# Kernel optimization log

Measured on AMD Instinct MI355X. Metric: run time of the kernel, lower is better.

The kernel has to match this reference:

```python
import jax, jax.numpy as jnp
import numpy as np

OFFSETS = (1, 2, 4, 8)
N, C, H, E = 256, 512, 256, 4


def _layer_norm(x, w, b, eps=1e-5):
    mu = x.mean(-1, keepdims=True)
    var = ((x - mu) ** 2).mean(-1, keepdims=True)
    return (x - mu) / jnp.sqrt(var + eps) * w + b


def _linear_init(key, fan_in, fan_out):
    k1, k2 = jax.random.split(key)
    bound = 1.0 / np.sqrt(fan_in)
    w = jax.random.uniform(k1, (fan_in, fan_out), jnp.float32, -bound, bound)
    b = jax.random.uniform(k2, (fan_out,), jnp.float32, -bound, bound)
    return w, b


def setup_inputs() -> dict:
    key = jax.random.key(0)
    ks = jax.random.split(key, 8)
    h = jax.random.normal(ks[0], (N, C, H), jnp.float32)
    xyz = jax.random.normal(ks[1], (N, C, 3), jnp.float32) * 10.0
    valid = jax.random.randint(ks[2], (N, C), 0, 2).astype(bool)
    # msg_mlp: Linear(2H+E -> 2H), GELU, Linear(2H -> H)
    w1, b1 = _linear_init(ks[3], 2 * H + E, 2 * H)
    w2, b2 = _linear_init(ks[4], 2 * H, H)
    # update ResidualMLP: LN(H), Linear(H -> 4H), GELU, Linear(4H -> H)
    u1, bu1 = _linear_init(ks[5], H, 4 * H)
    u2, bu2 = _linear_init(ks[6], 4 * H, H)
    return {
        "h": h, "xyz": xyz, "valid": valid,
        "ln_n_w": jnp.ones((H,), jnp.float32), "ln_n_b": jnp.zeros((H,), jnp.float32),
        "w1": w1, "b1": b1, "w2": w2, "b2": b2,
        "ln_u_w": jnp.ones((H,), jnp.float32), "ln_u_b": jnp.zeros((H,), jnp.float32),
        "u1": u1, "bu1": bu1, "u2": u2, "bu2": bu2,
    }


def _msg_mlp(x, w1, b1, w2, b2):
    y = jax.nn.gelu(x @ w1 + b1, approximate=False)
    return y @ w2 + b2


def reference(h, xyz, valid, ln_n_w, ln_n_b, w1, b1, w2, b2,
              ln_u_w, ln_u_b, u1, bu1, u2, bu2):
    n, c, hd = h.shape
    h_in = _layer_norm(h, ln_n_w, ln_n_b)
    valid_f = valid.astype(h.dtype)[..., None]  # [N, C, 1]
    agg = jnp.zeros_like(h_in)
    for off in OFFSETS:
        if off >= c:
            continue
        # dst = [0, c-off), src = [off, c)
        h_i = h_in[:, : c - off]
        h_j = h_in[:, off:]
        v = (valid[:, off:] & valid[:, : c - off]).astype(h.dtype)[..., None]
        delta = xyz[:, off:] - xyz[:, : c - off]  # xyz_j - xyz_i
        dist = jnp.maximum(jnp.linalg.norm(delta, axis=-1, keepdims=True), 1e-6)
        unit = delta / dist
        e_fwd = jnp.concatenate([unit, dist], axis=-1)
        msg_fwd = _msg_mlp(jnp.concatenate([h_i, h_j, e_fwd], axis=-1), w1, b1, w2, b2)
        agg = agg.at[:, : c - off].add(msg_fwd * v)
        e_rev = jnp.concatenate([-unit, dist], axis=-1)
        msg_rev = _msg_mlp(jnp.concatenate([h_j, h_i, e_rev], axis=-1), w1, b1, w2, b2)
        agg = agg.at[:, off:].add(msg_rev * v)
    h = h + agg * valid_f
    # ResidualMLP update
    hu = _layer_norm(h, ln_u_w, ln_u_b)
    hu = jax.nn.gelu(hu @ u1 + bu1, approximate=False) @ u2 + bu2
    h = (h + hu) * valid_f
    return h
```

## Files before the change

### kernel.cpp

```cpp
#include <hip/hip_runtime.h>
#include <stdint.h>

typedef unsigned short u16;
typedef __attribute__((ext_vector_type(8))) short short8v;
typedef __attribute__((ext_vector_type(4))) short short4v;
typedef __attribute__((ext_vector_type(4))) float f32x4;

#define CC 512
#define HD 256

__device__ __forceinline__ u16 f2bf(float f) {
  union { float f; uint32_t u; } v; v.f = f;
  return (u16)((v.u + 0x7FFFu + ((v.u >> 16) & 1u)) >> 16);
}
__device__ __forceinline__ float bf2f(u16 h) {
  union { uint32_t u; float f; } v; v.u = ((uint32_t)h) << 16;
  return v.f;
}
__device__ __forceinline__ float gelu_c(float x) {
  float x2 = x * x;
  float a  = x * fmaf(x2, 0.044715f, 1.0f);
  float t  = __builtin_amdgcn_exp2f(a * -2.3022118f);
  return x * __builtin_amdgcn_rcpf(1.0f + t);
}

__global__ void prep_weights(const float* __restrict__ w1, const float* __restrict__ w2,
                             const float* __restrict__ u1, const float* __restrict__ u2,
                             u16* __restrict__ ws) {
  int idx = blockIdx.x * blockDim.x + threadIdx.x;
  if (idx >= 917504) return;
  float val;
  if (idx < 131072)      { int n = idx >> 8, k = idx & 255; val = w1[k * 512 + n]; }
  else if (idx < 262144) { int i = idx - 131072, n = i >> 8, k = i & 255; val = w1[(256 + k) * 512 + n]; }
  else if (idx < 393216) { int i = idx - 262144, n = i >> 9, k = i & 511; val = w2[k * 256 + n]; }
  else if (idx < 655360) { int i = idx - 393216, n = i >> 8, k = i & 255; val = u1[k * 1024 + n]; }
  else                   { int i = idx - 655360, n = i >> 10, k = i & 1023; val = u2[k * 256 + n]; }
  ws[idx] = f2bf(val);
}

#define SPQ 520
#define SHS 264
#define Q_OFF   0
#define P_OFF   33280
#define H_OFF   49920
#define W1E_OFF 66816
#define B1_OFF  75008
#define EX_OFF  77056
#define NV_OFF  79616
#define STRIP_LDS 79680

__global__ __launch_bounds__(512) void strip_kernel(
    const float* __restrict__ hin, const float* __restrict__ xyz, const int* __restrict__ valid,
    const float* __restrict__ lnw, const float* __restrict__ lnb,
    const float* __restrict__ w1, const float* __restrict__ b1,
    const u16* __restrict__ WaT, const u16* __restrict__ WbT,
    const u16* __restrict__ W2T, const float* __restrict__ b2,
    float* __restrict__ out) {
  extern __shared__ char lds[];
  u16* sQ   = (u16*)(lds + Q_OFF);
  u16* sP   = (u16*)(lds + P_OFF);
  u16* sH   = (u16*)(lds + H_OFF);
  u16* sAct = (u16*)(lds + H_OFF);
  float* sW1e = (float*)(lds + W1E_OFF);
  float* sB1  = (float*)(lds + B1_OFF);
  float* sEx  = (float*)(lds + EX_OFF);
  float* sEy = sEx + 128; float* sEz = sEx + 256;
  float* sEd = sEx + 384; float* sV  = sEx + 512;
  float* sNV = (float*)(lds + NV_OFF);

  const int tid  = threadIdx.x;
  const int lane = tid & 63;
  const int wid  = tid >> 6;
  const int quad = lane >> 4;
  const int l16  = lane & 15;
  const int n    = blockIdx.y;
  const int c0   = blockIdx.x * 16;

  for (int i = tid; i < 2048; i += 512) sW1e[i] = w1[262144 + i];
  sB1[tid] = b1[tid];

  if (tid < 128) {
    const int p = tid >> 4, r = tid & 15;
    const int off = 1 << (p >> 1);
    const bool fwd = ((p & 1) == 0);
    const int c = c0 + r;
    const int other = fwd ? (c + off) : (c - off);
    const bool inb = (other >= 0) && (other < CC);
    const int oc = inb ? other : c;
    float vv = 0.f;
    if (inb && (valid[n * CC + c] != 0) && (valid[n * CC + oc] != 0)) vv = 1.f;
    const float* xo = xyz + (size_t)(n * CC + oc) * 3;
    const float* xc = xyz + (size_t)(n * CC + c) * 3;
    const float dx = xo[0] - xc[0], dy = xo[1] - xc[1], dz = xo[2] - xc[2];
    const float dist = fmaxf(sqrtf(dx*dx + dy*dy + dz*dz), 1e-6f);
    const float rin = 1.f / dist;
    sEx[tid] = dx * rin; sEy[tid] = dy * rin; sEz[tid] = dz * rin;
    sEd[tid] = dist; sV[tid] = vv;
  }

  for (int i = 0; i < 4; ++i) {
    const int r = wid * 4 + i;
    const int ch = c0 - 8 + r;
    float x0 = 0.f, x1 = 0.f, x2 = 0.f, x3 = 0.f;
    if (ch >= 0 && ch < CC) {
      const float* src = hin + (size_t)(n * CC + ch) * HD + lane * 4;
      x0 = src[0]; x1 = src[1]; x2 = src[2]; x3 = src[3];
    }
    float s = x0 + x1 + x2 + x3;
    float ss = x0*x0 + x1*x1 + x2*x2 + x3*x3;
    #pragma unroll
    for (int m = 1; m < 64; m <<= 1) { s += __shfl_xor(s, m, 64); ss += __shfl_xor(ss, m, 64); }
    const float mu = s * (1.f / 256.f);
    const float rstd = rsqrtf(ss * (1.f / 256.f) - mu * mu + 1e-5f);
    const int k4 = lane * 4;
    short4v pk;
    ((u16*)&pk)[0] = f2bf((x0 - mu) * rstd * lnw[k4 + 0] + lnb[k4 + 0]);
    ((u16*)&pk)[1] = f2bf((x1 - mu) * rstd * lnw[k4 + 1] + lnb[k4 + 1]);
    ((u16*)&pk)[2] = f2bf((x2 - mu) * rstd * lnw[k4 + 2] + lnb[k4 + 2]);
    ((u16*)&pk)[3] = f2bf((x3 - mu) * rstd * lnw[k4 + 3] + lnb[k4 + 3]);
    *(short4v*)&sH[r * SHS + k4] = pk;
  }
  __syncthreads();

  if (tid < 16) {
    float s = 0.f;
    #pragma unroll
    for (int p = 0; p < 8; ++p) s += sV[p * 16 + tid];
    sNV[tid] = s;
  }
  for (int nt = wid; nt < 32; nt += 8) {
    const int col = nt * 16 + l16;
    short8v bw[8];
    {
      const u16* bp = WaT + (size_t)col * 256;
      #pragma unroll
      for (int ks = 0; ks < 8; ++ks) bw[ks] = *(const short8v*)(bp + ks * 32 + quad * 8);
      const u16* ar = sH + (8 + l16) * SHS;
      f32x4 acc = {0.f, 0.f, 0.f, 0.f};
      #pragma unroll
      for (int ks = 0; ks < 8; ++ks)
        acc = __builtin_amdgcn_mfma_f32_16x16x32_bf16(*(const short8v*)(ar + ks * 32 + quad * 8), bw[ks], acc, 0, 0, 0);
      #pragma unroll
      for (int r = 0; r < 4; ++r) sP[(quad * 4 + r) * SPQ + col] = f2bf(acc[r]);
    }
    {
      const u16* bp = WbT + (size_t)col * 256;
      #pragma unroll
      for (int ks = 0; ks < 8; ++ks) bw[ks] = *(const short8v*)(bp + ks * 32 + quad * 8);
      #pragma unroll
      for (int mt = 0; mt < 2; ++mt) {
        const u16* ar = sH + (mt * 16 + l16) * SHS;
        f32x4 acc = {0.f, 0.f, 0.f, 0.f};
        #pragma unroll
        for (int ks = 0; ks < 8; ++ks)
          acc = __builtin_amdgcn_mfma_f32_16x16x32_bf16(*(const short8v*)(ar + ks * 32 + quad * 8), bw[ks], acc, 0, 0, 0);
        #pragma unroll
        for (int r = 0; r < 4; ++r) sQ[(mt * 16 + quad * 4 + r) * SPQ + col] = f2bf(acc[r]);
      }
    }
  }
  __syncthreads();

  const int row = tid >> 5;
  const int kl  = tid & 31;
  float accr[4][4];
  #pragma unroll
  for (int b = 0; b < 4; ++b)
    #pragma unroll
    for (int j = 0; j < 4; ++j) accr[b][j] = 0.f;
  short4v pp[4];
  {
    const u16* pr = sP + row * SPQ;
    #pragma unroll
    for (int b = 0; b < 4; ++b) pp[b] = *(const short4v*)(pr + kl * 4 + b * 128);
  }
  for (int pass = 0; pass < 8; ++pass) {
    const float vv = sV[pass * 16 + row];
    if (vv != 0.f) {
      const int off = 1 << (pass >> 1);
      const int doff = (pass & 1) ? -off : off;
      const float ex = sEx[pass * 16 + row], ey = sEy[pass * 16 + row];
      const float ez = sEz[pass * 16 + row], ed = sEd[pass * 16 + row];
      const u16* qr = sQ + (row + 8 + doff) * SPQ;
      #pragma unroll
      for (int b = 0; b < 4; ++b) {
        const int k0 = kl * 4 + b * 128;
        short4v qq = *(const short4v*)(qr + k0);
        const float4 we0 = *(const float4*)&sW1e[k0];
        const float4 we1 = *(const float4*)&sW1e[512 + k0];
        const float4 we2 = *(const float4*)&sW1e[1024 + k0];
        const float4 we3 = *(const float4*)&sW1e[1536 + k0];
        const float4 bb  = *(const float4*)&sB1[k0];
        #pragma unroll
        for (int j = 0; j < 4; ++j) {
          float pre = bf2f(((u16*)&pp[b])[j]) + bf2f(((u16*)&qq)[j])
                    + ex * ((const float*)&we0)[j] + ey * ((const float*)&we1)[j]
                    + ez * ((const float*)&we2)[j] + ed * ((const float*)&we3)[j]
                    + ((const float*)&bb)[j];
          accr[b][j] += gelu_c(pre);
        }
      }
    }
  }
  __syncthreads();
  {
    u16* aw = sAct + row * SPQ;
    #pragma unroll
    for (int b = 0; b < 4; ++b) {
      short4v pk;
      #pragma unroll
      for (int j = 0; j < 4; ++j) ((u16*)&pk)[j] = f2bf(accr[b][j]);
      *(short4v*)(aw + kl * 4 + b * 128) = pk;
    }
  }
  __syncthreads();

  {
    const int nt0 = wid * 2, nt1 = wid * 2 + 1;
    const u16* b0p = W2T + (size_t)(nt0 * 16 + l16) * 512;
    const u16* b1p = W2T + (size_t)(nt1 * 16 + l16) * 512;
    f32x4 a0 = {0.f, 0.f, 0.f, 0.f}, a1 = {0.f, 0.f, 0.f, 0.f};
    #pragma unroll
    for (int ks = 0; ks < 16; ++ks) {
      short8v a = *(const short8v*)(sAct + l16 * SPQ + ks * 32 + quad * 8);
      a0 = __builtin_amdgcn_mfma_f32_16x16x32_bf16(a, *(const short8v*)(b0p + ks * 32 + quad * 8), a0, 0, 0, 0);
      a1 = __builtin_amdgcn_mfma_f32_16x16x32_bf16(a, *(const short8v*)(b1p + ks * 32 + quad * 8), a1, 0, 0, 0);
    }
    #pragma unroll
    for (int t = 0; t < 2; ++t) {
      const f32x4 av = t ? a1 : a0;
      const int col = (t ? nt1 : nt0) * 16 + l16;
      const float b2v = b2[col];
      #pragma unroll
      for (int r = 0; r < 4; ++r) {
        const int rw = quad * 4 + r;
        const int gc = c0 + rw;
        const float vown = (valid[n * CC + gc] != 0) ? 1.f : 0.f;
        const size_t gi = (size_t)(n * CC + gc) * HD + col;
        out[gi] = hin[gi] + (av[r] + b2v * sNV[rw]) * vown;
      }
    }
  }
}

#define X_S 264
#define Y_S 520
#define UX_OFF 0
#define UY_OFF 16896
#define UPD_LDS 50176

__global__ __launch_bounds__(512) void update_kernel(
    const float* __restrict__ lnw, const float* __restrict__ lnb,
    const u16* __restrict__ U1T, const float* __restrict__ bu1,
    const u16* __restrict__ U2T, const float* __restrict__ bu2,
    const int* __restrict__ valid, float* __restrict__ out) {
  extern __shared__ char lds[];
  u16* sX = (u16*)(lds + UX_OFF);
  u16* sY = (u16*)(lds + UY_OFF);

  const int tid  = threadIdx.x;
  const int lane = tid & 63;
  const int wid  = tid >> 6;
  const int quad = lane >> 4;
  const int l16  = lane & 15;
  const int n    = blockIdx.y;
  const int c0   = blockIdx.x * 32;

  for (int i = 0; i < 4; ++i) {
    const int r = wid * 4 + i;
    const int k4 = lane * 4;
    const float* src = out + (size_t)(n * CC + c0 + r) * HD + k4;
    const float x0 = src[0], x1 = src[1], x2 = src[2], x3 = src[3];
    float s = x0 + x1 + x2 + x3;
    float ss = x0*x0 + x1*x1 + x2*x2 + x3*x3;
    #pragma unroll
    for (int m = 1; m < 64; m <<= 1) { s += __shfl_xor(s, m, 64); ss += __shfl_xor(ss, m, 64); }
    const float mu = s * (1.f / 256.f);
    const float rstd = rsqrtf(ss * (1.f / 256.f) - mu * mu + 1e-5f);
    short4v pk;
    ((u16*)&pk)[0] = f2bf((x0 - mu) * rstd * lnw[k4 + 0] + lnb[k4 + 0]);
    ((u16*)&pk)[1] = f2bf((x1 - mu) * rstd * lnw[k4 + 1] + lnb[k4 + 1]);
    ((u16*)&pk)[2] = f2bf((x2 - mu) * rstd * lnw[k4 + 2] + lnb[k4 + 2]);
    ((u16*)&pk)[3] = f2bf((x3 - mu) * rstd * lnw[k4 + 3] + lnb[k4 + 3]);
    *(short4v*)&sX[r * X_S + k4] = pk;
  }
  __syncthreads();

  const int nt0 = wid * 2, nt1 = wid * 2 + 1;
  f32x4 acc2[2][2];
  #pragma unroll
  for (int a = 0; a < 2; ++a)
    #pragma unroll
    for (int b = 0; b < 2; ++b) acc2[a][b] = (f32x4){0.f, 0.f, 0.f, 0.f};

  for (int half = 0; half < 2; ++half) {
    if (half) __syncthreads();
    for (int j = 0; j < 4; ++j) {
      const int nt = wid + j * 8;
      const int nrow = half * 512 + nt * 16 + l16;
      short8v bw[8];
      const u16* bp = U1T + (size_t)nrow * 256;
      #pragma unroll
      for (int ks = 0; ks < 8; ++ks) bw[ks] = *(const short8v*)(bp + ks * 32 + quad * 8);
      const float bv = bu1[nrow];
      #pragma unroll
      for (int mt = 0; mt < 2; ++mt) {
        const u16* ar = sX + (mt * 16 + l16) * X_S;
        f32x4 acc = {0.f, 0.f, 0.f, 0.f};
        #pragma unroll
        for (int ks = 0; ks < 8; ++ks)
          acc = __builtin_amdgcn_mfma_f32_16x16x32_bf16(*(const short8v*)(ar + ks * 32 + quad * 8), bw[ks], acc, 0, 0, 0);
        #pragma unroll
        for (int r = 0; r < 4; ++r)
          sY[(mt * 16 + quad * 4 + r) * Y_S + nt * 16 + l16] = f2bf(gelu_c(acc[r] + bv));
      }
    }
    __syncthreads();
    const u16* b0p = U2T + (size_t)(nt0 * 16 + l16) * 1024 + half * 512;
    const u16* b1p = U2T + (size_t)(nt1 * 16 + l16) * 1024 + half * 512;
    #pragma unroll
    for (int ks = 0; ks < 16; ++ks) {
      short8v aA = *(const short8v*)(sY + l16 * Y_S + ks * 32 + quad * 8);
      short8v aB = *(const short8v*)(sY + (16 + l16) * Y_S + ks * 32 + quad * 8);
      short8v b0 = *(const short8v*)(b0p + ks * 32 + quad * 8);
      short8v b1 = *(const short8v*)(b1p + ks * 32 + quad * 8);
      acc2[0][0] = __builtin_amdgcn_mfma_f32_16x16x32_bf16(aA, b0, acc2[0][0], 0, 0, 0);
      acc2[1][0] = __builtin_amdgcn_mfma_f32_16x16x32_bf16(aB, b0, acc2[1][0], 0, 0, 0);
      acc2[0][1] = __builtin_amdgcn_mfma_f32_16x16x32_bf16(aA, b1, acc2[0][1], 0, 0, 0);
      acc2[1][1] = __builtin_amdgcn_mfma_f32_16x16x32_bf16(aB, b1, acc2[1][1], 0, 0, 0);
    }
  }

  #pragma unroll
  for (int mt = 0; mt < 2; ++mt) {
    #pragma unroll
    for (int t = 0; t < 2; ++t) {
      const int col = (t ? nt1 : nt0) * 16 + l16;
      const float bv = bu2[col];
      #pragma unroll
      for (int r = 0; r < 4; ++r) {
        const int rw = mt * 16 + quad * 4 + r;
        const int gc = c0 + rw;
        const float vown = (valid[n * CC + gc] != 0) ? 1.f : 0.f;
        const size_t gi = (size_t)(n * CC + gc) * HD + col;
        out[gi] = (out[gi] + acc2[mt][t][r] + bv) * vown;
      }
    }
  }
}

extern "C" void kernel_launch(void* const* d_in, const int* in_sizes, int n_in,
                              void* d_out, int out_size, void* d_ws, size_t ws_size,
                              hipStream_t stream) {
  (void)in_sizes; (void)n_in; (void)out_size; (void)ws_size;
  const float* h     = (const float*)d_in[0];
  const float* xyz   = (const float*)d_in[1];
  const int*   valid = (const int*)d_in[2];
  const float* lnnw  = (const float*)d_in[3];
  const float* lnnb  = (const float*)d_in[4];
  const float* w1    = (const float*)d_in[5];
  const float* b1    = (const float*)d_in[6];
  const float* w2    = (const float*)d_in[7];
  const float* b2    = (const float*)d_in[8];
  const float* lnuw  = (const float*)d_in[9];
  const float* lnub  = (const float*)d_in[10];
  const float* u1    = (const float*)d_in[11];
  const float* bu1   = (const float*)d_in[12];
  const float* u2    = (const float*)d_in[13];
  const float* bu2   = (const float*)d_in[14];
  float* out = (float*)d_out;
  u16* ws = (u16*)d_ws;

  hipFuncSetAttribute(reinterpret_cast<const void*>(strip_kernel),
                      hipFuncAttributeMaxDynamicSharedMemorySize, STRIP_LDS);
  hipFuncSetAttribute(reinterpret_cast<const void*>(update_kernel),
                      hipFuncAttributeMaxDynamicSharedMemorySize, UPD_LDS);

  prep_weights<<<dim3(3584), dim3(256), 0, stream>>>(w1, w2, u1, u2, ws);
  strip_kernel<<<dim3(32, 256), dim3(512), STRIP_LDS, stream>>>(
      h, xyz, valid, lnnw, lnnb, w1, b1, ws, ws + 131072, ws + 262144, b2, out);
  update_kernel<<<dim3(16, 256), dim3(512), UPD_LDS, stream>>>(
      lnuw, lnub, ws + 393216, bu1, ws + 655360, bu2, valid, out);
}
```

Before: 1.511 ms.

## Fuse strip message kernel with residual MLP update kernel via LDS handoff

Merges the message-passing strip kernel and the residual-MLP update kernel into one kernel. The intermediate h is kept in LDS instead of being written to global memory and read back. The b1 bias is folded into the P projection, and edge weights are held in registers rather than LDS, which shrinks LDS use and targets 4 blocks per CU. The cost is that the update MLP now runs on 16-row tiles, so each U1/U2 weight fetch is reused across half as many rows, and register pressure rises.

```diff
diff --git a/kernel.cpp b/kernel.cpp
--- a/kernel.cpp
+++ b/kernel.cpp
@@ -40,30 +40,33 @@
 
 #define SPQ 520
 #define SHS 264
+#define OUTS 260
 #define Q_OFF   0
 #define P_OFF   33280
 #define H_OFF   49920
-#define W1E_OFF 66816
-#define B1_OFF  75008
-#define EX_OFF  77056
-#define NV_OFF  79616
-#define STRIP_LDS 79680
-
-__global__ __launch_bounds__(512) void strip_kernel(
+#define E_OFF   66816
+#define NV_OFF  69376
+#define FUSED_LDS 69440
+
+__global__ __launch_bounds__(512, 4) void fused_kernel(
     const float* __restrict__ hin, const float* __restrict__ xyz, const int* __restrict__ valid,
     const float* __restrict__ lnw, const float* __restrict__ lnb,
     const float* __restrict__ w1, const float* __restrict__ b1,
     const u16* __restrict__ WaT, const u16* __restrict__ WbT,
     const u16* __restrict__ W2T, const float* __restrict__ b2,
+    const float* __restrict__ lnuw, const float* __restrict__ lnub,
+    const u16* __restrict__ U1T, const float* __restrict__ bu1,
+    const u16* __restrict__ U2T, const float* __restrict__ bu2,
     float* __restrict__ out) {
   extern __shared__ char lds[];
   u16* sQ   = (u16*)(lds + Q_OFF);
   u16* sP   = (u16*)(lds + P_OFF);
   u16* sH   = (u16*)(lds + H_OFF);
   u16* sAct = (u16*)(lds + H_OFF);
-  float* sW1e = (float*)(lds + W1E_OFF);
-  float* sB1  = (float*)(lds + B1_OFF);
-  float* sEx  = (float*)(lds + EX_OFF);
+  float* sOut = (float*)(lds + P_OFF);
+  u16* sX   = (u16*)(lds + Q_OFF);
+  u16* sY   = (u16*)(lds + Q_OFF + 8448);
+  float* sEx = (float*)(lds + E_OFF);
   float* sEy = sEx + 128; float* sEz = sEx + 256;
   float* sEd = sEx + 384; float* sV  = sEx + 512;
   float* sNV = (float*)(lds + NV_OFF);
@@ -75,9 +78,7 @@
   const int l16  = lane & 15;
   const int n    = blockIdx.y;
   const int c0   = blockIdx.x * 16;
-
-  for (int i = tid; i < 2048; i += 512) sW1e[i] = w1[262144 + i];
-  sB1[tid] = b1[tid];
+  const int k4   = lane * 4;
 
   if (tid < 128) {
     const int p = tid >> 4, r = tid & 15;
@@ -98,27 +99,30 @@
     sEd[tid] = dist; sV[tid] = vv;
   }
 
-  for (int i = 0; i < 4; ++i) {
-    const int r = wid * 4 + i;
-    const int ch = c0 - 8 + r;
-    float x0 = 0.f, x1 = 0.f, x2 = 0.f, x3 = 0.f;
-    if (ch >= 0 && ch < CC) {
-      const float* src = hin + (size_t)(n * CC + ch) * HD + lane * 4;
-      x0 = src[0]; x1 = src[1]; x2 = src[2]; x3 = src[3];
-    }
-    float s = x0 + x1 + x2 + x3;
-    float ss = x0*x0 + x1*x1 + x2*x2 + x3*x3;
-    #pragma unroll
-    for (int m = 1; m < 64; m <<= 1) { s += __shfl_xor(s, m, 64); ss += __shfl_xor(ss, m, 64); }
-    const float mu = s * (1.f / 256.f);
-    const float rstd = rsqrtf(ss * (1.f / 256.f) - mu * mu + 1e-5f);
-    const int k4 = lane * 4;
-    short4v pk;
-    ((u16*)&pk)[0] = f2bf((x0 - mu) * rstd * lnw[k4 + 0] + lnb[k4 + 0]);
-    ((u16*)&pk)[1] = f2bf((x1 - mu) * rstd * lnw[k4 + 1] + lnb[k4 + 1]);
-    ((u16*)&pk)[2] = f2bf((x2 - mu) * rstd * lnw[k4 + 2] + lnb[k4 + 2]);
-    ((u16*)&pk)[3] = f2bf((x3 - mu) * rstd * lnw[k4 + 3] + lnb[k4 + 3]);
-    *(short4v*)&sH[r * SHS + k4] = pk;
+  {
+    const float4 lw = *(const float4*)&lnw[k4];
+    const float4 lb = *(const float4*)&lnb[k4];
+    for (int i = 0; i < 4; ++i) {
+      const int r = wid * 4 + i;
+      const int ch = c0 - 8 + r;
+      float x0 = 0.f, x1 = 0.f, x2 = 0.f, x3 = 0.f;
+      if (ch >= 0 && ch < CC) {
+        const float* src = hin + (size_t)(n * CC + ch) * HD + k4;
+        x0 = src[0]; x1 = src[1]; x2 = src[2]; x3 = src[3];
+      }
+      float s = x0 + x1 + x2 + x3;
+      float ss = x0*x0 + x1*x1 + x2*x2 + x3*x3;
+      #pragma unroll
+      for (int m = 1; m < 64; m <<= 1) { s += __shfl_xor(s, m, 64); ss += __shfl_xor(ss, m, 64); }
+      const float mu = s * (1.f / 256.f);
+      const float rstd = rsqrtf(ss * (1.f / 256.f) - mu * mu + 1e-5f);
+      short4v pk;
+      ((u16*)&pk)[0] = f2bf((x0 - mu) * rstd * lw.x + lb.x);
+      ((u16*)&pk)[1] = f2bf((x1 - mu) * rstd * lw.y + lb.y);
+      ((u16*)&pk)[2] = f2bf((x2 - mu) * rstd * lw.z + lb.z);
+      ((u16*)&pk)[3] = f2bf((x3 - mu) * rstd * lw.w + lb.w);
+      *(short4v*)&sH[r * SHS + k4] = pk;
+    }
   }
   __syncthreads();
 
@@ -140,8 +144,9 @@
       #pragma unroll
       for (int ks = 0; ks < 8; ++ks)
         acc = __builtin_amdgcn_mfma_f32_16x16x32_bf16(*(const short8v*)(ar + ks * 32 + quad * 8), bw[ks], acc, 0, 0, 0);
-      #pragma unroll
-      for (int r = 0; r < 4; ++r) sP[(quad * 4 + r) * SPQ + col] = f2bf(acc[r]);
+      const float bias = b1[col];
+      #pragma unroll
+      for (int r = 0; r < 4; ++r) sP[(quad * 4 + r) * SPQ + col] = f2bf(acc[r] + bias);
     }
     {
       const u16* bp = WbT + (size_t)col * 256;
@@ -163,47 +168,45 @@
 
   const int row = tid >> 5;
   const int kl  = tid & 31;
-  float accr[4][4];
-  #pragma unroll
-  for (int b = 0; b < 4; ++b)
-    #pragma unroll
-    for (int j = 0; j < 4; ++j) accr[b][j] = 0.f;
-  short4v pp[4];
   {
-    const u16* pr = sP + row * SPQ;
-    #pragma unroll
-    for (int b = 0; b < 4; ++b) pp[b] = *(const short4v*)(pr + kl * 4 + b * 128);
-  }
-  for (int pass = 0; pass < 8; ++pass) {
-    const float vv = sV[pass * 16 + row];
-    if (vv != 0.f) {
-      const int off = 1 << (pass >> 1);
-      const int doff = (pass & 1) ? -off : off;
-      const float ex = sEx[pass * 16 + row], ey = sEy[pass * 16 + row];
-      const float ez = sEz[pass * 16 + row], ed = sEd[pass * 16 + row];
-      const u16* qr = sQ + (row + 8 + doff) * SPQ;
-      #pragma unroll
-      for (int b = 0; b < 4; ++b) {
-        const int k0 = kl * 4 + b * 128;
-        short4v qq = *(const short4v*)(qr + k0);
-        const float4 we0 = *(const float4*)&sW1e[k0];
-        const float4 we1 = *(const float4*)&sW1e[512 + k0];
-        const float4 we2 = *(const float4*)&sW1e[1024 + k0];
-        const float4 we3 = *(const float4*)&sW1e[1536 + k0];
-        const float4 bb  = *(const float4*)&sB1[k0];
+    short4v pp[4];
+    float4 we[4][4];
+    #pragma unroll
+    for (int b = 0; b < 4; ++b) pp[b] = *(const short4v*)(sP + row * SPQ + kl * 4 + b * 128);
+    #pragma unroll
+    for (int d = 0; d < 4; ++d)
+      #pragma unroll
+      for (int b = 0; b < 4; ++b)
+        we[d][b] = *(const float4*)&w1[(size_t)(512 + d) * 512 + kl * 4 + b * 128];
+    float accr[4][4];
+    #pragma unroll
+    for (int b = 0; b < 4; ++b)
+      #pragma unroll
+      for (int j = 0; j < 4; ++j) accr[b][j] = 0.f;
+
+    for (int pass = 0; pass < 8; ++pass) {
+      const float vv = sV[pass * 16 + row];
+      if (vv != 0.f) {
+        const int off = 1 << (pass >> 1);
+        const int doff = (pass & 1) ? -off : off;
+        const float ex = sEx[pass * 16 + row], ey = sEy[pass * 16 + row];
+        const float ez = sEz[pass * 16 + row], ed = sEd[pass * 16 + row];
+        const u16* qr = sQ + (row + 8 + doff) * SPQ;
         #pragma unroll
-        for (int j = 0; j < 4; ++j) {
-          float pre = bf2f(((u16*)&pp[b])[j]) + bf2f(((u16*)&qq)[j])
-                    + ex * ((const float*)&we0)[j] + ey * ((const float*)&we1)[j]
-                    + ez * ((const float*)&we2)[j] + ed * ((const float*)&we3)[j]
-                    + ((const float*)&bb)[j];
-          accr[b][j] += gelu_c(pre);
+        for (int b = 0; b < 4; ++b) {
+          short4v qq = *(const short4v*)(qr + kl * 4 + b * 128);
+          #pragma unroll
+          for (int j = 0; j < 4; ++j) {
+            float et = ex * ((const float*)&we[0][b])[j];
+            et = fmaf(ey, ((const float*)&we[1][b])[j], et);
+            et = fmaf(ez, ((const float*)&we[2][b])[j], et);
+            et = fmaf(ed, ((const float*)&we[3][b])[j], et);
+            const float pre = bf2f(((const u16*)&pp[b])[j]) + bf2f(((const u16*)&qq)[j]) + et;
+            accr[b][j] += gelu_c(pre);
+          }
         }
       }
     }
-  }
-  __syncthreads();
-  {
     u16* aw = sAct + row * SPQ;
     #pragma unroll
     for (int b = 0; b < 4; ++b) {
@@ -215,8 +218,8 @@
   }
   __syncthreads();
 
+  const int nt0 = wid * 2, nt1 = wid * 2 + 1;
   {
-    const int nt0 = wid * 2, nt1 = wid * 2 + 1;
     const u16* b0p = W2T + (size_t)(nt0 * 16 + l16) * 512;
     const u16* b1p = W2T + (size_t)(nt1 * 16 + l16) * 512;
     f32x4 a0 = {0.f, 0.f, 0.f, 0.f}, a1 = {0.f, 0.f, 0.f, 0.f};
@@ -236,63 +239,39 @@
         const int rw = quad * 4 + r;
         const int gc = c0 + rw;
         const float vown = (valid[n * CC + gc] != 0) ? 1.f : 0.f;
-        const size_t gi = (size_t)(n * CC + gc) * HD + col;
-        out[gi] = hin[gi] + (av[r] + b2v * sNV[rw]) * vown;
+        const float hnew = hin[(size_t)(n * CC + gc) * HD + col] + (av[r] + b2v * sNV[rw]) * vown;
+        sOut[rw * OUTS + col] = hnew;
       }
     }
   }
-}
-
-#define X_S 264
-#define Y_S 520
-#define UX_OFF 0
-#define UY_OFF 16896
-#define UPD_LDS 50176
-
-__global__ __launch_bounds__(512) void update_kernel(
-    const float* __restrict__ lnw, const float* __restrict__ lnb,
-    const u16* __restrict__ U1T, const float* __restrict__ bu1,
-    const u16* __restrict__ U2T, const float* __restrict__ bu2,
-    const int* __restrict__ valid, float* __restrict__ out) {
-  extern __shared__ char lds[];
-  u16* sX = (u16*)(lds + UX_OFF);
-  u16* sY = (u16*)(lds + UY_OFF);
-
-  const int tid  = threadIdx.x;
-  const int lane = tid & 63;
-  const int wid  = tid >> 6;
-  const int quad = lane >> 4;
-  const int l16  = lane & 15;
-  const int n    = blockIdx.y;
-  const int c0   = blockIdx.x * 32;
-
-  for (int i = 0; i < 4; ++i) {
-    const int r = wid * 4 + i;
-    const int k4 = lane * 4;
-    const float* src = out + (size_t)(n * CC + c0 + r) * HD + k4;
-    const float x0 = src[0], x1 = src[1], x2 = src[2], x3 = src[3];
-    float s = x0 + x1 + x2 + x3;
-    float ss = x0*x0 + x1*x1 + x2*x2 + x3*x3;
-    #pragma unroll
-    for (int m = 1; m < 64; m <<= 1) { s += __shfl_xor(s, m, 64); ss += __shfl_xor(ss, m, 64); }
-    const float mu = s * (1.f / 256.f);
-    const float rstd = rsqrtf(ss * (1.f / 256.f) - mu * mu + 1e-5f);
-    short4v pk;
-    ((u16*)&pk)[0] = f2bf((x0 - mu) * rstd * lnw[k4 + 0] + lnb[k4 + 0]);
-    ((u16*)&pk)[1] = f2bf((x1 - mu) * rstd * lnw[k4 + 1] + lnb[k4 + 1]);
-    ((u16*)&pk)[2] = f2bf((x2 - mu) * rstd * lnw[k4 + 2] + lnb[k4 + 2]);
-    ((u16*)&pk)[3] = f2bf((x3 - mu) * rstd * lnw[k4 + 3] + lnb[k4 + 3]);
-    *(short4v*)&sX[r * X_S + k4] = pk;
-  }
-  __syncthreads();
-
-  const int nt0 = wid * 2, nt1 = wid * 2 + 1;
-  f32x4 acc2[2][2];
-  #pragma unroll
-  for (int a = 0; a < 2; ++a)
-    #pragma unroll
-    for (int b = 0; b < 2; ++b) acc2[a][b] = (f32x4){0.f, 0.f, 0.f, 0.f};
-
+  __syncthreads();
+
+  {
+    const float4 uw = *(const float4*)&lnuw[k4];
+    const float4 ub = *(const float4*)&lnub[k4];
+    #pragma unroll
+    for (int i = 0; i < 2; ++i) {
+      const int r = wid * 2 + i;
+      const float4 x = *(const float4*)&sOut[r * OUTS + k4];
+      float s = x.x + x.y + x.z + x.w;
+      float ss = x.x*x.x + x.y*x.y + x.z*x.z + x.w*x.w;
+      #pragma unroll
+      for (int m = 1; m < 64; m <<= 1) { s += __shfl_xor(s, m, 64); ss += __shfl_xor(ss, m, 64); }
+      const float mu = s * (1.f / 256.f);
+      const float rstd = rsqrtf(ss * (1.f / 256.f) - mu * mu + 1e-5f);
+      short4v pk;
+      ((u16*)&pk)[0] = f2bf((x.x - mu) * rstd * uw.x + ub.x);
+      ((u16*)&pk)[1] = f2bf((x.y - mu) * rstd * uw.y + ub.y);
+      ((u16*)&pk)[2] = f2bf((x.z - mu) * rstd * uw.z + ub.z);
+      ((u16*)&pk)[3] = f2bf((x.w - mu) * rstd * uw.w + ub.w);
+      *(short4v*)&sX[r * 264 + k4] = pk;
+    }
+  }
+  __syncthreads();
+
+  f32x4 acc2[2];
+  acc2[0] = (f32x4){0.f, 0.f, 0.f, 0.f};
+  acc2[1] = (f32x4){0.f, 0.f, 0.f, 0.f};
   for (int half = 0; half < 2; ++half) {
     if (half) __syncthreads();
     for (int j = 0; j < 4; ++j) {
@@ -303,48 +282,36 @@
       #pragma unroll
       for (int ks = 0; ks < 8; ++ks) bw[ks] = *(const short8v*)(bp + ks * 32 + quad * 8);
       const float bv = bu1[nrow];
-      #pragma unroll
-      for (int mt = 0; mt < 2; ++mt) {
-        const u16* ar = sX + (mt * 16 + l16) * X_S;
-        f32x4 acc = {0.f, 0.f, 0.f, 0.f};
-        #pragma unroll
-        for (int ks = 0; ks < 8; ++ks)
-          acc = __builtin_amdgcn_mfma_f32_16x16x32_bf16(*(const short8v*)(ar + ks * 32 + quad * 8), bw[ks], acc, 0, 0, 0);
-        #pragma unroll
-        for (int r = 0; r < 4; ++r)
-          sY[(mt * 16 + quad * 4 + r) * Y_S + nt * 16 + l16] = f2bf(gelu_c(acc[r] + bv));
-      }
+      const u16* ar = sX + l16 * 264;
+      f32x4 acc = {0.f, 0.f, 0.f, 0.f};
+      #pragma unroll
+      for (int ks = 0; ks < 8; ++ks)
+        acc = __builtin_amdgcn_mfma_f32_16x16x32_bf16(*(const short8v*)(ar + ks * 32 + quad * 8), bw[ks], acc, 0, 0, 0);
+      #pragma unroll
+      for (int r = 0; r < 4; ++r)
+        sY[(quad * 4 + r) * 520 + nt * 16 + l16] = f2bf(gelu_c(acc[r] + bv));
     }
     __syncthreads();
-    const u16* b0p = U2T + (size_t)(nt0 * 16 + l16) * 1024 + half * 512;
-    const u16* b1p = U2T + (size_t)(nt1 * 16 + l16) * 1024 + half * 512;
+    const u16* c0p = U2T + (size_t)(nt0 * 16 + l16) * 1024 + half * 512;
+    const u16* c1p = U2T + (size_t)(nt1 * 16 + l16) * 1024 + half * 512;
     #pragma unroll
     for (int ks = 0; ks < 16; ++ks) {
-      short8v aA = *(const short8v*)(sY + l16 * Y_S + ks * 32 + quad * 8);
-      short8v aB = *(const short8v*)(sY + (16 + l16) * Y_S + ks * 32 + quad * 8);
-      short8v b0 = *(const short8v*)(b0p + ks * 32 + quad * 8);
-      short8v b1 = *(const short8v*)(b1p + ks * 32 + quad * 8);
-      acc2[0][0] = __builtin_amdgcn_mfma_f32_16x16x32_bf16(aA, b0, acc2[0][0], 0, 0, 0);
-      acc2[1][0] = __builtin_amdgcn_mfma_f32_16x16x32_bf16(aB, b0, acc2[1][0], 0, 0, 0);
-      acc2[0][1] = __builtin_amdgcn_mfma_f32_16x16x32_bf16(aA, b1, acc2[0][1], 0, 0, 0);
-      acc2[1][1] = __builtin_amdgcn_mfma_f32_16x16x32_bf16(aB, b1, acc2[1][1], 0, 0, 0);
+      short8v a = *(const short8v*)(sY + l16 * 520 + ks * 32 + quad * 8);
+      acc2[0] = __builtin_amdgcn_mfma_f32_16x16x32_bf16(a, *(const short8v*)(c0p + ks * 32 + quad * 8), acc2[0], 0, 0, 0);
+      acc2[1] = __builtin_amdgcn_mfma_f32_16x16x32_bf16(a, *(const short8v*)(c1p + ks * 32 + quad * 8), acc2[1], 0, 0, 0);
     }
   }
 
   #pragma unroll
-  for (int mt = 0; mt < 2; ++mt) {
-    #pragma unroll
-    for (int t = 0; t < 2; ++t) {
-      const int col = (t ? nt1 : nt0) * 16 + l16;
-      const float bv = bu2[col];
-      #pragma unroll
-      for (int r = 0; r < 4; ++r) {
-        const int rw = mt * 16 + quad * 4 + r;
-        const int gc = c0 + rw;
-        const float vown = (valid[n * CC + gc] != 0) ? 1.f : 0.f;
-        const size_t gi = (size_t)(n * CC + gc) * HD + col;
-        out[gi] = (out[gi] + acc2[mt][t][r] + bv) * vown;
-      }
+  for (int t = 0; t < 2; ++t) {
+    const int col = (t ? nt1 : nt0) * 16 + l16;
+    const float bv = bu2[col];
+    #pragma unroll
+    for (int r = 0; r < 4; ++r) {
+      const int rw = quad * 4 + r;
+      const int gc = c0 + rw;
+      const float vown = (valid[n * CC + gc] != 0) ? 1.f : 0.f;
+      out[(size_t)(n * CC + gc) * HD + col] = (sOut[rw * OUTS + col] + acc2[t][r] + bv) * vown;
     }
   }
 }
@@ -371,14 +338,12 @@
   float* out = (float*)d_out;
   u16* ws = (u16*)d_ws;
 
-  hipFuncSetAttribute(reinterpret_cast<const void*>(strip_kernel),
-                      hipFuncAttributeMaxDynamicSharedMemorySize, STRIP_LDS);
-  hipFuncSetAttribute(reinterpret_cast<const void*>(update_kernel),
-                      hipFuncAttributeMaxDynamicSharedMemorySize, UPD_LDS);
+  hipFuncSetAttribute(reinterpret_cast<const void*>(fused_kernel),
+                      hipFuncAttributeMaxDynamicSharedMemorySize, FUSED_LDS);
 
   prep_weights<<<dim3(3584), dim3(256), 0, stream>>>(w1, w2, u1, u2, ws);
-  strip_kernel<<<dim3(32, 256), dim3(512), STRIP_LDS, stream>>>(
-      h, xyz, valid, lnnw, lnnb, w1, b1, ws, ws + 131072, ws + 262144, b2, out);
-  update_kernel<<<dim3(16, 256), dim3(512), UPD_LDS, stream>>>(
-      lnuw, lnub, ws + 393216, bu1, ws + 655360, bu2, valid, out);
-}
+  fused_kernel<<<dim3(32, 256), dim3(512), FUSED_LDS, stream>>>(
+      h, xyz, valid, lnnw, lnnb, w1, b1,
+      ws, ws + 131072, ws + 262144, b2,
+      lnuw, lnub, ws + 393216, bu1, ws + 655360, bu2, out);
+}
```

New measurement: 1.972 ms. 1.31x slower.

## Keep P projection in registers and cut LDS to raise occupancy in both kernels

Applied to the files above, without the earlier changes.

The strip kernel no longer stages the P projection, edge weights and bias in LDS. It keeps the P accumulator (with bias folded in) and the edge weights in registers, and the elementwise message stage now uses the MFMA output layout. The update kernel splits the 1024-wide hidden dimension into four chunks of 256 instead of two of 512, which shrinks the Y buffer. Both kernels use less LDS and get occupancy hints in launch_bounds, aiming at more resident blocks. The trade-off is higher register pressure, per-row validity checks inside the pass loop, more barriers in the update kernel, and scattered u16 LDS stores.

```diff
diff --git a/kernel.cpp b/kernel.cpp
--- a/kernel.cpp
+++ b/kernel.cpp
@@ -41,15 +41,12 @@
 #define SPQ 520
 #define SHS 264
 #define Q_OFF   0
-#define P_OFF   33280
-#define H_OFF   49920
-#define W1E_OFF 66816
-#define B1_OFF  75008
-#define EX_OFF  77056
-#define NV_OFF  79616
-#define STRIP_LDS 79680
-
-__global__ __launch_bounds__(512) void strip_kernel(
+#define H_OFF   33280
+#define E_OFF   50176
+#define NV_OFF  52736
+#define STRIP_LDS 52800
+
+__global__ __launch_bounds__(512, 6) void strip_kernel(
     const float* __restrict__ hin, const float* __restrict__ xyz, const int* __restrict__ valid,
     const float* __restrict__ lnw, const float* __restrict__ lnb,
     const float* __restrict__ w1, const float* __restrict__ b1,
@@ -58,12 +55,9 @@
     float* __restrict__ out) {
   extern __shared__ char lds[];
   u16* sQ   = (u16*)(lds + Q_OFF);
-  u16* sP   = (u16*)(lds + P_OFF);
   u16* sH   = (u16*)(lds + H_OFF);
   u16* sAct = (u16*)(lds + H_OFF);
-  float* sW1e = (float*)(lds + W1E_OFF);
-  float* sB1  = (float*)(lds + B1_OFF);
-  float* sEx  = (float*)(lds + EX_OFF);
+  float* sEx = (float*)(lds + E_OFF);
   float* sEy = sEx + 128; float* sEz = sEx + 256;
   float* sEd = sEx + 384; float* sV  = sEx + 512;
   float* sNV = (float*)(lds + NV_OFF);
@@ -75,9 +69,7 @@
   const int l16  = lane & 15;
   const int n    = blockIdx.y;
   const int c0   = blockIdx.x * 16;
-
-  for (int i = tid; i < 2048; i += 512) sW1e[i] = w1[262144 + i];
-  sB1[tid] = b1[tid];
+  const int k4   = lane * 4;
 
   if (tid < 128) {
     const int p = tid >> 4, r = tid & 15;
@@ -98,27 +90,30 @@
     sEd[tid] = dist; sV[tid] = vv;
   }
 
-  for (int i = 0; i < 4; ++i) {
-    const int r = wid * 4 + i;
-    const int ch = c0 - 8 + r;
-    float x0 = 0.f, x1 = 0.f, x2 = 0.f, x3 = 0.f;
-    if (ch >= 0 && ch < CC) {
-      const float* src = hin + (size_t)(n * CC + ch) * HD + lane * 4;
-      x0 = src[0]; x1 = src[1]; x2 = src[2]; x3 = src[3];
-    }
-    float s = x0 + x1 + x2 + x3;
-    float ss = x0*x0 + x1*x1 + x2*x2 + x3*x3;
-    #pragma unroll
-    for (int m = 1; m < 64; m <<= 1) { s += __shfl_xor(s, m, 64); ss += __shfl_xor(ss, m, 64); }
-    const float mu = s * (1.f / 256.f);
-    const float rstd = rsqrtf(ss * (1.f / 256.f) - mu * mu + 1e-5f);
-    const int k4 = lane * 4;
-    short4v pk;
-    ((u16*)&pk)[0] = f2bf((x0 - mu) * rstd * lnw[k4 + 0] + lnb[k4 + 0]);
-    ((u16*)&pk)[1] = f2bf((x1 - mu) * rstd * lnw[k4 + 1] + lnb[k4 + 1]);
-    ((u16*)&pk)[2] = f2bf((x2 - mu) * rstd * lnw[k4 + 2] + lnb[k4 + 2]);
-    ((u16*)&pk)[3] = f2bf((x3 - mu) * rstd * lnw[k4 + 3] + lnb[k4 + 3]);
-    *(short4v*)&sH[r * SHS + k4] = pk;
+  {
+    const float4 lw = *(const float4*)&lnw[k4];
+    const float4 lb = *(const float4*)&lnb[k4];
+    for (int i = 0; i < 4; ++i) {
+      const int r = wid * 4 + i;
+      const int ch = c0 - 8 + r;
+      float x0 = 0.f, x1 = 0.f, x2 = 0.f, x3 = 0.f;
+      if (ch >= 0 && ch < CC) {
+        const float* src = hin + (size_t)(n * CC + ch) * HD + k4;
+        x0 = src[0]; x1 = src[1]; x2 = src[2]; x3 = src[3];
+      }
+      float s = x0 + x1 + x2 + x3;
+      float ss = x0*x0 + x1*x1 + x2*x2 + x3*x3;
+      #pragma unroll
+      for (int m = 1; m < 64; m <<= 1) { s += __shfl_xor(s, m, 64); ss += __shfl_xor(ss, m, 64); }
+      const float mu = s * (1.f / 256.f);
+      const float rstd = rsqrtf(ss * (1.f / 256.f) - mu * mu + 1e-5f);
+      short4v pk;
+      ((u16*)&pk)[0] = f2bf((x0 - mu) * rstd * lw.x + lb.x);
+      ((u16*)&pk)[1] = f2bf((x1 - mu) * rstd * lw.y + lb.y);
+      ((u16*)&pk)[2] = f2bf((x2 - mu) * rstd * lw.z + lb.z);
+      ((u16*)&pk)[3] = f2bf((x3 - mu) * rstd * lw.w + lb.w);
+      *(short4v*)&sH[r * SHS + k4] = pk;
+    }
   }
   __syncthreads();
 
@@ -128,7 +123,11 @@
     for (int p = 0; p < 8; ++p) s += sV[p * 16 + tid];
     sNV[tid] = s;
   }
-  for (int nt = wid; nt < 32; nt += 8) {
+
+  float pAcc[4][4];
+  #pragma unroll
+  for (int j = 0; j < 4; ++j) {
+    const int nt = wid + j * 8;
     const int col = nt * 16 + l16;
     short8v bw[8];
     {
@@ -140,8 +139,9 @@
       #pragma unroll
       for (int ks = 0; ks < 8; ++ks)
         acc = __builtin_amdgcn_mfma_f32_16x16x32_bf16(*(const short8v*)(ar + ks * 32 + quad * 8), bw[ks], acc, 0, 0, 0);
-      #pragma unroll
-      for (int r = 0; r < 4; ++r) sP[(quad * 4 + r) * SPQ + col] = f2bf(acc[r]);
+      const float bias = b1[col];
+      #pragma unroll
+      for (int r = 0; r < 4; ++r) pAcc[j][r] = acc[r] + bias;
     }
     {
       const u16* bp = WbT + (size_t)col * 256;
@@ -159,59 +159,54 @@
       }
     }
   }
+  float we[4][4];
+  #pragma unroll
+  for (int d = 0; d < 4; ++d)
+    #pragma unroll
+    for (int j = 0; j < 4; ++j)
+      we[d][j] = w1[(size_t)(512 + d) * 512 + (wid + j * 8) * 16 + l16];
   __syncthreads();
 
-  const int row = tid >> 5;
-  const int kl  = tid & 31;
   float accr[4][4];
   #pragma unroll
-  for (int b = 0; b < 4; ++b)
-    #pragma unroll
-    for (int j = 0; j < 4; ++j) accr[b][j] = 0.f;
-  short4v pp[4];
-  {
-    const u16* pr = sP + row * SPQ;
-    #pragma unroll
-    for (int b = 0; b < 4; ++b) pp[b] = *(const short4v*)(pr + kl * 4 + b * 128);
-  }
+  for (int j = 0; j < 4; ++j)
+    #pragma unroll
+    for (int r = 0; r < 4; ++r) accr[j][r] = 0.f;
+
   for (int pass = 0; pass < 8; ++pass) {
-    const float vv = sV[pass * 16 + row];
-    if (vv != 0.f) {
+    float vvr[4];
+    #pragma unroll
+    for (int r = 0; r < 4; ++r) vvr[r] = sV[pass * 16 + quad * 4 + r];
+    if (vvr[0] + vvr[1] + vvr[2] + vvr[3] != 0.f) {
       const int off = 1 << (pass >> 1);
       const int doff = (pass & 1) ? -off : off;
-      const float ex = sEx[pass * 16 + row], ey = sEy[pass * 16 + row];
-      const float ez = sEz[pass * 16 + row], ed = sEd[pass * 16 + row];
-      const u16* qr = sQ + (row + 8 + doff) * SPQ;
-      #pragma unroll
-      for (int b = 0; b < 4; ++b) {
-        const int k0 = kl * 4 + b * 128;
-        short4v qq = *(const short4v*)(qr + k0);
-        const float4 we0 = *(const float4*)&sW1e[k0];
-        const float4 we1 = *(const float4*)&sW1e[512 + k0];
-        const float4 we2 = *(const float4*)&sW1e[1024 + k0];
-        const float4 we3 = *(const float4*)&sW1e[1536 + k0];
-        const float4 bb  = *(const float4*)&sB1[k0];
-        #pragma unroll
-        for (int j = 0; j < 4; ++j) {
-          float pre = bf2f(((u16*)&pp[b])[j]) + bf2f(((u16*)&qq)[j])
-                    + ex * ((const float*)&we0)[j] + ey * ((const float*)&we1)[j]
-                    + ez * ((const float*)&we2)[j] + ed * ((const float*)&we3)[j]
-                    + ((const float*)&bb)[j];
-          accr[b][j] += gelu_c(pre);
+      #pragma unroll
+      for (int r = 0; r < 4; ++r) {
+        if (vvr[r] != 0.f) {
+          const int row = quad * 4 + r;
+          const float ex = sEx[pass * 16 + row], ey = sEy[pass * 16 + row];
+          const float ez = sEz[pass * 16 + row], ed = sEd[pass * 16 + row];
+          const u16* qr = sQ + (row + 8 + doff) * SPQ;
+          #pragma unroll
+          for (int j = 0; j < 4; ++j) {
+            const int col = (wid + j * 8) * 16 + l16;
+            float et = ex * we[0][j];
+            et = fmaf(ey, we[1][j], et);
+            et = fmaf(ez, we[2][j], et);
+            et = fmaf(ed, we[3][j], et);
+            const float pre = pAcc[j][r] + bf2f(qr[col]) + et;
+            accr[j][r] += gelu_c(pre);
+          }
         }
       }
     }
   }
-  __syncthreads();
-  {
-    u16* aw = sAct + row * SPQ;
-    #pragma unroll
-    for (int b = 0; b < 4; ++b) {
-      short4v pk;
-      #pragma unroll
-      for (int j = 0; j < 4; ++j) ((u16*)&pk)[j] = f2bf(accr[b][j]);
-      *(short4v*)(aw + kl * 4 + b * 128) = pk;
-    }
+  #pragma unroll
+  for (int r = 0; r < 4; ++r) {
+    u16* aw = sAct + (quad * 4 + r) * SPQ;
+    #pragma unroll
+    for (int j = 0; j < 4; ++j)
+      aw[(wid + j * 8) * 16 + l16] = f2bf(accr[j][r]);
   }
   __syncthreads();
 
@@ -244,12 +239,12 @@
 }
 
 #define X_S 264
-#define Y_S 520
+#define Y_S 264
 #define UX_OFF 0
 #define UY_OFF 16896
-#define UPD_LDS 50176
-
-__global__ __launch_bounds__(512) void update_kernel(
+#define UPD_LDS 33792
+
+__global__ __launch_bounds__(512, 8) void update_kernel(
     const float* __restrict__ lnw, const float* __restrict__ lnb,
     const u16* __restrict__ U1T, const float* __restrict__ bu1,
     const u16* __restrict__ U2T, const float* __restrict__ bu2,
@@ -265,39 +260,41 @@
   const int l16  = lane & 15;
   const int n    = blockIdx.y;
   const int c0   = blockIdx.x * 32;
-
-  for (int i = 0; i < 4; ++i) {
-    const int r = wid * 4 + i;
-    const int k4 = lane * 4;
-    const float* src = out + (size_t)(n * CC + c0 + r) * HD + k4;
-    const float x0 = src[0], x1 = src[1], x2 = src[2], x3 = src[3];
-    float s = x0 + x1 + x2 + x3;
-    float ss = x0*x0 + x1*x1 + x2*x2 + x3*x3;
-    #pragma unroll
-    for (int m = 1; m < 64; m <<= 1) { s += __shfl_xor(s, m, 64); ss += __shfl_xor(ss, m, 64); }
-    const float mu = s * (1.f / 256.f);
-    const float rstd = rsqrtf(ss * (1.f / 256.f) - mu * mu + 1e-5f);
-    short4v pk;
-    ((u16*)&pk)[0] = f2bf((x0 - mu) * rstd * lnw[k4 + 0] + lnb[k4 + 0]);
-    ((u16*)&pk)[1] = f2bf((x1 - mu) * rstd * lnw[k4 + 1] + lnb[k4 + 1]);
-    ((u16*)&pk)[2] = f2bf((x2 - mu) * rstd * lnw[k4 + 2] + lnb[k4 + 2]);
-    ((u16*)&pk)[3] = f2bf((x3 - mu) * rstd * lnw[k4 + 3] + lnb[k4 + 3]);
-    *(short4v*)&sX[r * X_S + k4] = pk;
+  const int k4   = lane * 4;
+
+  {
+    const float4 lw = *(const float4*)&lnw[k4];
+    const float4 lb = *(const float4*)&lnb[k4];
+    for (int i = 0; i < 4; ++i) {
+      const int r = wid * 4 + i;
+      const float* src = out + (size_t)(n * CC + c0 + r) * HD + k4;
+      const float x0 = src[0], x1 = src[1], x2 = src[2], x3 = src[3];
+      float s = x0 + x1 + x2 + x3;
+      float ss = x0*x0 + x1*x1 + x2*x2 + x3*x3;
+      #pragma unroll
+      for (int m = 1; m < 64; m <<= 1) { s += __shfl_xor(s, m, 64); ss += __shfl_xor(ss, m, 64); }
+      const float mu = s * (1.f / 256.f);
+      const float rstd = rsqrtf(ss * (1.f / 256.f) - mu * mu + 1e-5f);
+      short4v pk;
+      ((u16*)&pk)[0] = f2bf((x0 - mu) * rstd * lw.x + lb.x);
+      ((u16*)&pk)[1] = f2bf((x1 - mu) * rstd * lw.y + lb.y);
+      ((u16*)&pk)[2] = f2bf((x2 - mu) * rstd * lw.z + lb.z);
+      ((u16*)&pk)[3] = f2bf((x3 - mu) * rstd * lw.w + lb.w);
+      *(short4v*)&sX[r * X_S + k4] = pk;
+    }
   }
   __syncthreads();
 
-  const int nt0 = wid * 2, nt1 = wid * 2 + 1;
-  f32x4 acc2[2][2];
-  #pragma unroll
-  for (int a = 0; a < 2; ++a)
-    #pragma unroll
-    for (int b = 0; b < 2; ++b) acc2[a][b] = (f32x4){0.f, 0.f, 0.f, 0.f};
-
-  for (int half = 0; half < 2; ++half) {
-    if (half) __syncthreads();
-    for (int j = 0; j < 4; ++j) {
-      const int nt = wid + j * 8;
-      const int nrow = half * 512 + nt * 16 + l16;
+  f32x4 acc2[4];
+  #pragma unroll
+  for (int i = 0; i < 4; ++i) acc2[i] = (f32x4){0.f, 0.f, 0.f, 0.f};
+
+  for (int q = 0; q < 4; ++q) {
+    if (q) __syncthreads();
+    #pragma unroll
+    for (int t = 0; t < 2; ++t) {
+      const int nt = wid * 2 + t;
+      const int nrow = q * 256 + nt * 16 + l16;
       short8v bw[8];
       const u16* bp = U1T + (size_t)nrow * 256;
       #pragma unroll
@@ -316,34 +313,36 @@
       }
     }
     __syncthreads();
-    const u16* b0p = U2T + (size_t)(nt0 * 16 + l16) * 1024 + half * 512;
-    const u16* b1p = U2T + (size_t)(nt1 * 16 + l16) * 1024 + half * 512;
-    #pragma unroll
-    for (int ks = 0; ks < 16; ++ks) {
-      short8v aA = *(const short8v*)(sY + l16 * Y_S + ks * 32 + quad * 8);
-      short8v aB = *(const short8v*)(sY + (16 + l16) * Y_S + ks * 32 + quad * 8);
-      short8v b0 = *(const short8v*)(b0p + ks * 32 + quad * 8);
-      short8v b1 = *(const short8v*)(b1p + ks * 32 + quad * 8);
-      acc2[0][0] = __builtin_amdgcn_mfma_f32_16x16x32_bf16(aA, b0, acc2[0][0], 0, 0, 0);
-      acc2[1][0] = __builtin_amdgcn_mfma_f32_16x16x32_bf16(aB, b0, acc2[1][0], 0, 0, 0);
-      acc2[0][1] = __builtin_amdgcn_mfma_f32_16x16x32_bf16(aA, b1, acc2[0][1], 0, 0, 0);
-      acc2[1][1] = __builtin_amdgcn_mfma_f32_16x16x32_bf16(aB, b1, acc2[1][1], 0, 0, 0);
-    }
-  }
-
-  #pragma unroll
-  for (int mt = 0; mt < 2; ++mt) {
     #pragma unroll
     for (int t = 0; t < 2; ++t) {
-      const int col = (t ? nt1 : nt0) * 16 + l16;
-      const float bv = bu2[col];
+      const int nt = wid * 2 + t;
+      short8v cw[8];
+      const u16* cp = U2T + (size_t)(nt * 16 + l16) * 1024 + q * 256;
+      #pragma unroll
+      for (int ks = 0; ks < 8; ++ks) cw[ks] = *(const short8v*)(cp + ks * 32 + quad * 8);
+      #pragma unroll
+      for (int mt = 0; mt < 2; ++mt) {
+        const u16* ar = sY + (mt * 16 + l16) * Y_S;
+        #pragma unroll
+        for (int ks = 0; ks < 8; ++ks)
+          acc2[t * 2 + mt] = __builtin_amdgcn_mfma_f32_16x16x32_bf16(*(const short8v*)(ar + ks * 32 + quad * 8), cw[ks], acc2[t * 2 + mt], 0, 0, 0);
+      }
+    }
+  }
+
+  #pragma unroll
+  for (int t = 0; t < 2; ++t) {
+    const int col = (wid * 2 + t) * 16 + l16;
+    const float bv = bu2[col];
+    #pragma unroll
+    for (int mt = 0; mt < 2; ++mt) {
       #pragma unroll
       for (int r = 0; r < 4; ++r) {
         const int rw = mt * 16 + quad * 4 + r;
         const int gc = c0 + rw;
         const float vown = (valid[n * CC + gc] != 0) ? 1.f : 0.f;
         const size_t gi = (size_t)(n * CC + gc) * HD + col;
-        out[gi] = (out[gi] + acc2[mt][t][r] + bv) * vown;
+        out[gi] = (out[gi] + acc2[t * 2 + mt][r] + bv) * vown;
       }
     }
   }
@@ -378,7 +377,8 @@
 
   prep_weights<<<dim3(3584), dim3(256), 0, stream>>>(w1, w2, u1, u2, ws);
   strip_kernel<<<dim3(32, 256), dim3(512), STRIP_LDS, stream>>>(
-      h, xyz, valid, lnnw, lnnb, w1, b1, ws, ws + 131072, ws + 262144, b2, out);
+      h, xyz, valid, lnnw, lnnb, w1, b1,
+      ws, ws + 131072, ws + 262144, b2, out);
   update_kernel<<<dim3(16, 256), dim3(512), UPD_LDS, stream>>>(
       lnuw, lnub, ws + 393216, bu1, ws + 655360, bu2, valid, out);
 }
```

Result: faster. 1.449 ms (-4.1%).
